# Kernel optimization log

Hardware: AMD Instinct MI355X
Metric: run time of the kernel (lower is better)

Reference implementation:

```python
import jax, jax.numpy as jnp
import numpy as np

B, T, TM, D, H, FF = 4, 1024, 1024, 1024, 16, 4096
HS = D // H
EPS = 1e-5


def _layer_norm(x, g, b):
    m = jnp.mean(x, axis=-1, keepdims=True)
    v = jnp.mean(jnp.square(x - m), axis=-1, keepdims=True)
    return (x - m) / jnp.sqrt(v + EPS) * g + b


def _mha(q_in, k_in, v_in, wq, bq, wk, bk, wv, bv, wo, bo):
    b, t, c = q_in.shape
    tm = k_in.shape[1]
    q = (q_in @ wq + bq).reshape(b, t, H, HS).transpose(0, 2, 1, 3)   # [b,h,t,hs]
    k = (k_in @ wk + bk).reshape(b, tm, H, HS).transpose(0, 2, 1, 3)  # [b,h,tm,hs]
    v = (v_in @ wv + bv).reshape(b, tm, H, HS).transpose(0, 2, 1, 3)
    att = jnp.einsum('bhtd,bhsd->bhts', q, k) * (1.0 / np.sqrt(HS))
    att = jax.nn.softmax(att, axis=-1)                                # [b,h,t,tm]
    y = jnp.einsum('bhts,bhsd->bhtd', att, v)
    y = y.transpose(0, 2, 1, 3).reshape(b, t, c)
    y = y @ wo + bo
    return y, att.mean(axis=1)                                        # attn avg over heads


def setup_inputs() -> dict:
    key = jax.random.key(0)
    ks = jax.random.split(key, 32)
    s = 0.02
    w = lambda k, shape: (jax.random.normal(k, shape, jnp.float32) * s)
    inp = {
        'tgt': jax.random.normal(ks[0], (B, T, D), jnp.float32),
        'memory': jax.random.normal(ks[1], (B, TM, D), jnp.float32),
        # self-attention params
        'sa_wq': w(ks[2], (D, D)), 'sa_bq': jnp.zeros((D,), jnp.float32),
        'sa_wk': w(ks[3], (D, D)), 'sa_bk': jnp.zeros((D,), jnp.float32),
        'sa_wv': w(ks[4], (D, D)), 'sa_bv': jnp.zeros((D,), jnp.float32),
        'sa_wo': w(ks[5], (D, D)), 'sa_bo': jnp.zeros((D,), jnp.float32),
        # cross-attention params
        'ca_wq': w(ks[6], (D, D)), 'ca_bq': jnp.zeros((D,), jnp.float32),
        'ca_wk': w(ks[7], (D, D)), 'ca_bk': jnp.zeros((D,), jnp.float32),
        'ca_wv': w(ks[8], (D, D)), 'ca_bv': jnp.zeros((D,), jnp.float32),
        'ca_wo': w(ks[9], (D, D)), 'ca_bo': jnp.zeros((D,), jnp.float32),
        # FFN
        'w1': w(ks[10], (D, FF)), 'b1': jnp.zeros((FF,), jnp.float32),
        'w2': w(ks[11], (FF, D)), 'b2': jnp.zeros((D,), jnp.float32),
        # LayerNorms
        'ln1_g': jnp.ones((D,), jnp.float32), 'ln1_b': jnp.zeros((D,), jnp.float32),
        'ln2_g': jnp.ones((D,), jnp.float32), 'ln2_b': jnp.zeros((D,), jnp.float32),
        'ln3_g': jnp.ones((D,), jnp.float32), 'ln3_b': jnp.zeros((D,), jnp.float32),
    }
    return inp


def reference(tgt, memory,
              sa_wq, sa_bq, sa_wk, sa_bk, sa_wv, sa_bv, sa_wo, sa_bo,
              ca_wq, ca_bq, ca_wk, ca_bk, ca_wv, ca_bv, ca_wo, ca_bo,
              w1, b1, w2, b2,
              ln1_g, ln1_b, ln2_g, ln2_b, ln3_g, ln3_b):
    x = tgt
    tmp, _ = _mha(x, x, x, sa_wq, sa_bq, sa_wk, sa_bk, sa_wv, sa_bv, sa_wo, sa_bo)
    x = _layer_norm(x + tmp, ln1_g, ln1_b)
    tmp, attention = _mha(x, memory, memory,
                          ca_wq, ca_bq, ca_wk, ca_bk, ca_wv, ca_bv, ca_wo, ca_bo)
    x = _layer_norm(x + tmp, ln2_g, ln2_b)
    tmp = jax.nn.relu(x @ w1 + b1) @ w2 + b2
    x = _layer_norm(x + tmp, ln3_g, ln3_b)
    return x, attention
```

## Files before the change

kernel.cpp:

```cpp
#include <hip/hip_runtime.h>
#include <hip/hip_bf16.h>
#include <cstdint>
#include <cstddef>

using u16 = unsigned short;
typedef __attribute__((ext_vector_type(4))) float f32x4;
typedef __attribute__((ext_vector_type(8))) short bf16x8;
typedef __attribute__((ext_vector_type(4))) short bf16x4;

constexpr int Bc = 4, Tc = 1024, TMc = 1024, Dc = 1024, Hc = 16, HSc = 64, FFc = 4096;
constexpr int BT = Bc * Tc;

struct Ptr4 { u16* p0; u16* p1; u16* p2; u16* p3; };

__device__ __forceinline__ u16 f2bf(float f) {
  union { float f; uint32_t u; } v; v.f = f;
  uint32_t u = v.u;
  u += 0x7fffu + ((u >> 16) & 1u);
  return (u16)(u >> 16);
}
__device__ __forceinline__ float b2f(u16 u) {
  union { float f; uint32_t u32; } v; v.u32 = (uint32_t)u << 16; return v.f;
}

__device__ __forceinline__ bf16x8 cat8(bf16x4 lo, bf16x4 hi) {
  bf16x8 r;
  r[0] = lo[0]; r[1] = lo[1]; r[2] = lo[2]; r[3] = lo[3];
  r[4] = hi[0]; r[5] = hi[1]; r[6] = hi[2]; r[7] = hi[3];
  return r;
}

__device__ __forceinline__ void gload16(const u16* g, u16* l) {
  __builtin_amdgcn_global_load_lds((const __attribute__((address_space(1))) void*)g,
                                   (__attribute__((address_space(3))) void*)l, 16, 0, 0);
}

__global__ __launch_bounds__(256)
void tconv(const float* __restrict__ in, u16* __restrict__ outp, int K, int N)
{
  __shared__ u16 tile[64][65];
  const int tx = threadIdx.x & 15, ty = threadIdx.x >> 4;
  const int kb = blockIdx.y * 64, nb = blockIdx.x * 64;
  #pragma unroll
  for (int i = 0; i < 4; ++i) {
    const int r = ty + i * 16;
    const float4 v = *(const float4*)(in + (size_t)(kb + r) * N + nb + tx * 4);
    tile[r][tx * 4 + 0] = f2bf(v.x);
    tile[r][tx * 4 + 1] = f2bf(v.y);
    tile[r][tx * 4 + 2] = f2bf(v.z);
    tile[r][tx * 4 + 3] = f2bf(v.w);
  }
  __syncthreads();
  #pragma unroll
  for (int i = 0; i < 4; ++i) {
    const int n = ty + i * 16;
    bf16x4 o;
    o[0] = (short)tile[tx * 4 + 0][n];
    o[1] = (short)tile[tx * 4 + 1][n];
    o[2] = (short)tile[tx * 4 + 2][n];
    o[3] = (short)tile[tx * 4 + 3][n];
    *(bf16x4*)(outp + (size_t)(nb + n) * K + kb + tx * 4) = o;
  }
}

__global__ __launch_bounds__(256)
void cvt_bf16(const float* __restrict__ in, u16* __restrict__ outp, int n4)
{
  const int i = blockIdx.x * 256 + threadIdx.x;
  if (i < n4) {
    const float4 v = ((const float4*)in)[i];
    bf16x4 o;
    o[0] = (short)f2bf(v.x); o[1] = (short)f2bf(v.y);
    o[2] = (short)f2bf(v.z); o[3] = (short)f2bf(v.w);
    ((bf16x4*)outp)[i] = o;
  }
}

template<int MODE, int BMv, int DEPTH>
__global__ __launch_bounds__((BMv == 256) ? 512 : 256)
void gemm_bt(const u16* __restrict__ A, const u16* __restrict__ Bt,
             const float* __restrict__ bias, const float* __restrict__ resid,
             void* __restrict__ outp, int M, int N, int K, int Kch, Ptr4 P)
{
  constexpr int BM = BMv, BN = 128, BK = 32;
  constexpr int NTHR = (BM == 256) ? 512 : 256;
  constexpr int RPC = NTHR / 4;
  constexpr int ACALLS = BM / RPC;
  constexpr int BCALLS = BN / RPC;
  constexpr int CALLS = ACALLS + BCALLS;
  constexpr int NB = DEPTH + 1;
  __shared__ __align__(16) u16 As[NB][BM * BK];
  __shared__ __align__(16) u16 Bs[NB][BN * BK];
  const int tid = threadIdx.x;
  const int lane = tid & 63, w = tid >> 6;
  const int wr = w >> 1, wc = w & 1;
  const int hi4 = lane >> 4, lr = lane & 15;

  const int nwg = gridDim.x;
  const int GX = N / BN;
  const int bid0 = (int)blockIdx.x;
  const int L = (bid0 & 7) * (nwg >> 3) + (bid0 >> 3);
  const int bandw = 8 * GX;
  const int band = L / bandw;
  const int rem = L - band * bandw;
  const int m0 = (band * 8 + (rem & 7)) * BM;
  const int n0 = (rem >> 3) * BN;

  const int k0 = (MODE == 3) ? (int)blockIdx.y * Kch : 0;

  const int srow = tid >> 2;
  const int gslot = (tid & 3) ^ ((srow >> 1) & 3);
  const u16* ga = A  + (size_t)(m0 + srow) * K + k0 + gslot * 8;
  const u16* gb = Bt + (size_t)(n0 + srow) * K + k0 + gslot * 8;
  const int wofs = w * 512;
  const int cswz = (lr >> 1) & 3;

  auto stage = [&](int buf, int kt) {
    #pragma unroll
    for (int j = 0; j < ACALLS; ++j)
      gload16(ga + (size_t)j * RPC * K + kt, &As[buf][j * NTHR * 8 + wofs]);
    #pragma unroll
    for (int j = 0; j < BCALLS; ++j)
      gload16(gb + (size_t)j * RPC * K + kt, &Bs[buf][j * NTHR * 8 + wofs]);
  };

  f32x4 acc[4][4] = {};
  const int nt = Kch / BK;

  #pragma unroll
  for (int p = 0; p < DEPTH; ++p)
    if (p < nt) stage(p % NB, p * BK);

  int cur = 0;
  for (int t = 0; t < nt; ++t) {
    {
      const int ahead = nt - 1 - t;
      const int cap = (ahead < DEPTH - 1 ? ahead : DEPTH - 1) * CALLS;
      switch (cap) {
        case 0:  asm volatile("s_waitcnt vmcnt(0)"  ::: "memory"); break;
        case 3:  asm volatile("s_waitcnt vmcnt(3)"  ::: "memory"); break;
        case 4:  asm volatile("s_waitcnt vmcnt(4)"  ::: "memory"); break;
        case 8:  asm volatile("s_waitcnt vmcnt(8)"  ::: "memory"); break;
        default: asm volatile("s_waitcnt vmcnt(12)" ::: "memory"); break;
      }
    }
    __builtin_amdgcn_s_barrier();
    __builtin_amdgcn_sched_barrier(0);

    if (t + DEPTH < nt) {
      int b2 = cur + DEPTH; if (b2 >= NB) b2 -= NB;
      stage(b2, (t + DEPTH) * BK);
    }

    bf16x8 af[4], bfr[4];
    #pragma unroll
    for (int mb = 0; mb < 4; ++mb)
      af[mb] = *(const bf16x8*)&As[cur][(wr * 64 + mb * 16 + lr) * BK + (hi4 ^ cswz) * 8];
    #pragma unroll
    for (int nb = 0; nb < 4; ++nb)
      bfr[nb] = *(const bf16x8*)&Bs[cur][(wc * 64 + nb * 16 + lr) * BK + (hi4 ^ cswz) * 8];
    #pragma unroll
    for (int mb = 0; mb < 4; ++mb)
      #pragma unroll
      for (int nb = 0; nb < 4; ++nb)
        acc[mb][nb] = __builtin_amdgcn_mfma_f32_16x16x32_bf16(af[mb], bfr[nb], acc[mb][nb], 0, 0, 0);

    ++cur; if (cur == NB) cur = 0;
  }

  const int orow = m0 + wr * 64 + 4 * hi4;
  const int ocol = n0 + wc * 64 + lr;

  if (MODE == 1) {
    #pragma unroll
    for (int nb = 0; nb < 4; ++nb) {
      const int c = ocol + nb * 16;
      const float bv = bias ? bias[c] : 0.0f;
      #pragma unroll
      for (int mb = 0; mb < 4; ++mb) {
        #pragma unroll
        for (int r = 0; r < 4; ++r) {
          const size_t idx = (size_t)(orow + mb * 16 + r) * N + c;
          ((float*)outp)[idx] = acc[mb][nb][r] + bv + resid[idx];
        }
      }
    }
  } else {
    __syncthreads();
    u16* eb = &Bs[0][0] + w * 1088;
    u16* pout_;
    if (MODE == 3) {
      const int sk = blockIdx.y;
      pout_ = (sk == 0) ? P.p0 : (sk == 1) ? P.p1 : (sk == 2) ? P.p2 : P.p3;
    } else {
      pout_ = (u16*)outp;
    }
    const int r2 = lane >> 3;
    const int c2 = (lane & 7) * 8;
    #pragma unroll
    for (int mb = 0; mb < 4; ++mb) {
      #pragma unroll
      for (int nb = 0; nb < 4; ++nb) {
        const int c = ocol + nb * 16;
        const float bv = (MODE != 3 && bias) ? bias[c] : 0.0f;
        #pragma unroll
        for (int r = 0; r < 4; ++r) {
          float v = acc[mb][nb][r] + bv;
          if (MODE == 2) v = fmaxf(v, 0.0f);
          eb[(4 * hi4 + r) * 68 + nb * 16 + lr] = f2bf(v);
        }
      }
      #pragma unroll
      for (int pass = 0; pass < 2; ++pass) {
        const int rr = pass * 8 + r2;
        const bf16x8 vv = *(const bf16x8*)&eb[rr * 68 + c2];
        *(bf16x8*)&pout_[(size_t)(m0 + wr * 64 + mb * 16 + rr) * N + n0 + wc * 64 + c2] = vv;
      }
    }
  }
}

__global__ __launch_bounds__(256)
void flash_attn(const u16* __restrict__ Q, const u16* __restrict__ Kb,
                const u16* __restrict__ Vb, u16* __restrict__ Y,
                float* __restrict__ Mout, float* __restrict__ Lout,
                int qstr, int kstr)
{
  constexpr int LDK = 72;
  __shared__ __align__(16) u16 Ks[64 * LDK];
  __shared__ __align__(16) u16 Vt[64 * LDK];
  const int tid = threadIdx.x, lane = tid & 63, w = tid >> 6;
  const int hi4 = lane >> 4, lr = lane & 15;
  const int bh = blockIdx.y, b = bh >> 4, h = bh & 15;
  const int q0 = blockIdx.x * 64 + w * 16;

  bf16x8 qf[2];
  {
    const u16* qp = Q + ((size_t)(b * Tc + q0 + lr)) * qstr + h * HSc;
    #pragma unroll
    for (int ks = 0; ks < 2; ++ks)
      qf[ks] = cat8(*(const bf16x4*)(qp + ks * 32 + 4 * hi4),
                    *(const bf16x4*)(qp + ks * 32 + 16 + 4 * hi4));
  }

  float m_run = -1e30f, l_run = 0.0f;
  f32x4 o[4] = {};

  const int krow = tid >> 3, kcol = (tid & 7) * 8;
  const int vs = tid >> 4, vd = (tid & 15) * 4;
  const int vswz = 4 * (tid & 15);

  for (int s0 = 0; s0 < TMc; s0 += 64) {
    const u16* kp = Kb + ((size_t)(b * TMc + s0 + krow)) * kstr + h * HSc + kcol;
    *(bf16x8*)&Ks[krow * LDK + kcol]        = *(const bf16x8*)kp;
    *(bf16x8*)&Ks[(krow + 32) * LDK + kcol] = *(const bf16x8*)(kp + (size_t)32 * kstr);
    #pragma unroll
    for (int rr = 0; rr < 4; ++rr) {
      const int ss = vs + rr * 16;
      bf16x4 vv = *(const bf16x4*)(Vb + ((size_t)(b * TMc + s0 + ss)) * kstr + h * HSc + vd);
      const int sc_ = ss ^ vswz;
      Vt[(vd + 0) * LDK + sc_] = (u16)vv[0];
      Vt[(vd + 1) * LDK + sc_] = (u16)vv[1];
      Vt[(vd + 2) * LDK + sc_] = (u16)vv[2];
      Vt[(vd + 3) * LDK + sc_] = (u16)vv[3];
    }
    __syncthreads();

    f32x4 st[4];
    #pragma unroll
    for (int kb2 = 0; kb2 < 4; ++kb2) {
      f32x4 a = {};
      #pragma unroll
      for (int ks = 0; ks < 2; ++ks) {
        const u16* p = &Ks[(kb2 * 16 + lr) * LDK + ks * 32 + 4 * hi4];
        bf16x8 kf = cat8(*(const bf16x4*)p, *(const bf16x4*)(p + 16));
        a = __builtin_amdgcn_mfma_f32_16x16x32_bf16(kf, qf[ks], a, 0, 0, 0);
      }
      st[kb2] = a;
    }

    float cmax = -1e30f;
    #pragma unroll
    for (int kb2 = 0; kb2 < 4; ++kb2)
      #pragma unroll
      for (int r = 0; r < 4; ++r) {
        st[kb2][r] *= 0.125f;
        cmax = fmaxf(cmax, st[kb2][r]);
      }
    cmax = fmaxf(cmax, __shfl_xor(cmax, 16));
    cmax = fmaxf(cmax, __shfl_xor(cmax, 32));
    const float m_new = fmaxf(m_run, cmax);
    const float sc = __expf(m_run - m_new);
    float psum = 0.0f;
    #pragma unroll
    for (int kb2 = 0; kb2 < 4; ++kb2)
      #pragma unroll
      for (int r = 0; r < 4; ++r) {
        const float e = __expf(st[kb2][r] - m_new);
        st[kb2][r] = e;
        psum += e;
      }
    psum += __shfl_xor(psum, 16);
    psum += __shfl_xor(psum, 32);
    l_run = l_run * sc + psum;
    m_run = m_new;

    #pragma unroll
    for (int r = 0; r < 4; ++r) {
      const float osc = __shfl(sc, 4 * hi4 + r);
      #pragma unroll
      for (int nb = 0; nb < 4; ++nb) o[nb][r] *= osc;
    }

    bf16x8 pa[2];
    #pragma unroll
    for (int ks = 0; ks < 2; ++ks) {
      bf16x8 t;
      #pragma unroll
      for (int i = 0; i < 4; ++i) t[i]     = (short)f2bf(st[2 * ks + 0][i]);
      #pragma unroll
      for (int i = 0; i < 4; ++i) t[4 + i] = (short)f2bf(st[2 * ks + 1][i]);
      pa[ks] = t;
    }
    #pragma unroll
    for (int nb = 0; nb < 4; ++nb) {
      const int row = nb * 16 + lr;
      const int g = 4 * (row >> 2);
      #pragma unroll
      for (int ks = 0; ks < 2; ++ks) {
        const int c0 = (ks * 32 + 4 * hi4) ^ g;
        const int c1 = (ks * 32 + 16 + 4 * hi4) ^ g;
        bf16x8 vf = cat8(*(const bf16x4*)&Vt[row * LDK + c0],
                         *(const bf16x4*)&Vt[row * LDK + c1]);
        o[nb] = __builtin_amdgcn_mfma_f32_16x16x32_bf16(pa[ks], vf, o[nb], 0, 0, 0);
      }
    }
    __syncthreads();
  }

  #pragma unroll
  for (int r = 0; r < 4; ++r) {
    const float li = 1.0f / __shfl(l_run, 4 * hi4 + r);
    const size_t yr = ((size_t)(b * Tc + q0 + 4 * hi4 + r)) * Dc + h * HSc;
    #pragma unroll
    for (int nb = 0; nb < 4; ++nb)
      Y[yr + nb * 16 + lr] = f2bf(o[nb][r] * li);
  }
  if (Mout != nullptr && lane < 16) {
    Mout[(size_t)bh * Tc + q0 + lr] = m_run;
    Lout[(size_t)bh * Tc + q0 + lr] = l_run;
  }
}

__global__ __launch_bounds__(256)
void attn_avg(const u16* __restrict__ Q, const u16* __restrict__ Kb,
              const float* __restrict__ Mws, const float* __restrict__ Lws,
              float* __restrict__ outp, int qstr, int kstr)
{
  __shared__ __align__(16) u16 Ks[2][64 * 64];
  __shared__ __align__(16) float avg[64 * 68];
  const int tid = threadIdx.x, lane = tid & 63, w = tid >> 6;
  const int hi4 = lane >> 4, lr = lane & 15;
  const int b = blockIdx.z, qt = blockIdx.y, scn = blockIdx.x;
  const int q0 = qt * 64 + w * 16;
  const int s0 = scn * 64;

  const int srow = w * 8 + (lane >> 3);
  const int scol = ((lane & 7) ^ (lane >> 3)) * 8;
  const u16* kg = Kb + ((size_t)(b * TMc + s0 + srow)) * kstr + scol;
  const size_t skip32 = (size_t)32 * kstr;

  auto stage = [&](int buf, int h) {
    const u16* g = kg + h * HSc;
    gload16(g,          &Ks[buf][w * 512]);
    gload16(g + skip32, &Ks[buf][2048 + w * 512]);
  };

  float acc[4][4] = {};
  const int rsw = lr & 7;

  stage(0, 0);
  #pragma unroll 1
  for (int h = 0; h < Hc; ++h) {
    const int cur = h & 1;
    __syncthreads();
    if (h + 1 < Hc) stage(cur ^ 1, h + 1);

    const u16* qp = Q + ((size_t)(b * Tc + q0 + lr)) * qstr + h * HSc;
    const bf16x8 qf0 = *(const bf16x8*)(qp + 8 * hi4);
    const bf16x8 qf1 = *(const bf16x8*)(qp + 32 + 8 * hi4);
    const float mh = Mws[(size_t)(b * Hc + h) * Tc + q0 + lr];
    const float li = 1.0f / Lws[(size_t)(b * Hc + h) * Tc + q0 + lr];

    #pragma unroll
    for (int kb2 = 0; kb2 < 4; ++kb2) {
      const int row = kb2 * 16 + lr;
      const bf16x8 kf0 = *(const bf16x8*)&Ks[cur][row * 64 + ((hi4     ) ^ rsw) * 8];
      const bf16x8 kf1 = *(const bf16x8*)&Ks[cur][row * 64 + ((hi4 + 4) ^ rsw) * 8];
      f32x4 a = {};
      a = __builtin_amdgcn_mfma_f32_16x16x32_bf16(kf0, qf0, a, 0, 0, 0);
      a = __builtin_amdgcn_mfma_f32_16x16x32_bf16(kf1, qf1, a, 0, 0, 0);
      #pragma unroll
      for (int r = 0; r < 4; ++r)
        acc[kb2][r] += __expf(a[r] * 0.125f - mh) * li;
    }
  }

  __syncthreads();
  #pragma unroll
  for (int kb2 = 0; kb2 < 4; ++kb2)
    #pragma unroll
    for (int r = 0; r < 4; ++r)
      avg[(w * 16 + lr) * 68 + kb2 * 16 + 4 * hi4 + r] = acc[kb2][r] * (1.0f / Hc);
  __syncthreads();
  const int row = tid >> 2, col = (tid & 3) * 16;
  float* gp = outp + ((size_t)(b * Tc + qt * 64 + row)) * TMc + s0 + col;
  #pragma unroll
  for (int j = 0; j < 4; ++j)
    *(f32x4*)(gp + j * 4) = *(const f32x4*)&avg[row * 68 + col + j * 4];
}

__global__ __launch_bounds__(256)
void add_ln(const float* __restrict__ in, const float* __restrict__ g,
            const float* __restrict__ bb, float* __restrict__ outf,
            u16* __restrict__ outb)
{
  __shared__ float red1[4];
  __shared__ float red2[4];
  const int tid = threadIdx.x, lane = tid & 63, w = tid >> 6;
  const size_t row = blockIdx.x;
  float4 v = ((const float4*)(in + row * Dc))[tid];
  float s = v.x + v.y + v.z + v.w;
  #pragma unroll
  for (int o = 32; o >= 1; o >>= 1) s += __shfl_xor(s, o);
  if (lane == 0) red1[w] = s;
  __syncthreads();
  s = red1[0] + red1[1] + red1[2] + red1[3];
  const float mean = s * (1.0f / Dc);
  const float dx = v.x - mean, dy = v.y - mean, dz = v.z - mean, dw = v.w - mean;
  float s2 = dx * dx + dy * dy + dz * dz + dw * dw;
  #pragma unroll
  for (int o = 32; o >= 1; o >>= 1) s2 += __shfl_xor(s2, o);
  if (lane == 0) red2[w] = s2;
  __syncthreads();
  s2 = red2[0] + red2[1] + red2[2] + red2[3];
  const float rstd = rsqrtf(s2 * (1.0f / Dc) + 1e-5f);
  const float4 gv = ((const float4*)g)[tid];
  const float4 bv = ((const float4*)bb)[tid];
  float4 o4;
  o4.x = dx * rstd * gv.x + bv.x;
  o4.y = dy * rstd * gv.y + bv.y;
  o4.z = dz * rstd * gv.z + bv.z;
  o4.w = dw * rstd * gv.w + bv.w;
  ((float4*)(outf + row * Dc))[tid] = o4;
  if (outb != nullptr) {
    bf16x4 ob;
    ob[0] = (short)f2bf(o4.x); ob[1] = (short)f2bf(o4.y);
    ob[2] = (short)f2bf(o4.z); ob[3] = (short)f2bf(o4.w);
    *(bf16x4*)(outb + row * Dc + (size_t)tid * 4) = ob;
  }
}

__global__ __launch_bounds__(256)
void add_ln4(const u16* __restrict__ p0, const u16* __restrict__ p1,
             const u16* __restrict__ p2, const u16* __restrict__ p3,
             const float* __restrict__ bias2, const float* __restrict__ resid,
             const float* __restrict__ g, const float* __restrict__ bb,
             float* __restrict__ outf)
{
  __shared__ float red1[4];
  __shared__ float red2[4];
  const int tid = threadIdx.x, lane = tid & 63, w = tid >> 6;
  const size_t row = blockIdx.x;
  const size_t base = row * Dc + (size_t)tid * 4;
  const bf16x4 a0 = *(const bf16x4*)(p0 + base);
  const bf16x4 a1 = *(const bf16x4*)(p1 + base);
  const bf16x4 a2 = *(const bf16x4*)(p2 + base);
  const bf16x4 a3 = *(const bf16x4*)(p3 + base);
  const float4 rv = ((const float4*)(resid + row * Dc))[tid];
  const float4 b2 = ((const float4*)bias2)[tid];
  float4 v;
  v.x = b2f((u16)a0[0]) + b2f((u16)a1[0]) + b2f((u16)a2[0]) + b2f((u16)a3[0]) + b2.x + rv.x;
  v.y = b2f((u16)a0[1]) + b2f((u16)a1[1]) + b2f((u16)a2[1]) + b2f((u16)a3[1]) + b2.y + rv.y;
  v.z = b2f((u16)a0[2]) + b2f((u16)a1[2]) + b2f((u16)a2[2]) + b2f((u16)a3[2]) + b2.z + rv.z;
  v.w = b2f((u16)a0[3]) + b2f((u16)a1[3]) + b2f((u16)a2[3]) + b2f((u16)a3[3]) + b2.w + rv.w;
  float s = v.x + v.y + v.z + v.w;
  #pragma unroll
  for (int o = 32; o >= 1; o >>= 1) s += __shfl_xor(s, o);
  if (lane == 0) red1[w] = s;
  __syncthreads();
  s = red1[0] + red1[1] + red1[2] + red1[3];
  const float mean = s * (1.0f / Dc);
  const float dx = v.x - mean, dy = v.y - mean, dz = v.z - mean, dw = v.w - mean;
  float s2 = dx * dx + dy * dy + dz * dz + dw * dw;
  #pragma unroll
  for (int o = 32; o >= 1; o >>= 1) s2 += __shfl_xor(s2, o);
  if (lane == 0) red2[w] = s2;
  __syncthreads();
  s2 = red2[0] + red2[1] + red2[2] + red2[3];
  const float rstd = rsqrtf(s2 * (1.0f / Dc) + 1e-5f);
  const float4 gv = ((const float4*)g)[tid];
  const float4 bv = ((const float4*)bb)[tid];
  float4 o4;
  o4.x = dx * rstd * gv.x + bv.x;
  o4.y = dy * rstd * gv.y + bv.y;
  o4.z = dz * rstd * gv.z + bv.z;
  o4.w = dw * rstd * gv.w + bv.w;
  ((float4*)(outf + row * Dc))[tid] = o4;
}

extern "C" void kernel_launch(void* const* d_in, const int* in_sizes, int n_in,
                              void* d_out, int out_size, void* d_ws, size_t ws_size,
                              hipStream_t stream)
{
  (void)in_sizes; (void)n_in; (void)out_size; (void)ws_size;
  const float* tgt = (const float*)d_in[0];
  const float* mem = (const float*)d_in[1];
  const float* Wf[10]   = { (const float*)d_in[2],  (const float*)d_in[4],  (const float*)d_in[6],  (const float*)d_in[8],
                            (const float*)d_in[10], (const float*)d_in[12], (const float*)d_in[14], (const float*)d_in[16],
                            (const float*)d_in[18], (const float*)d_in[20] };
  const float* bias_[10]= { (const float*)d_in[3],  (const float*)d_in[5],  (const float*)d_in[7],  (const float*)d_in[9],
                            (const float*)d_in[11], (const float*)d_in[13], (const float*)d_in[15], (const float*)d_in[17],
                            (const float*)d_in[19], (const float*)d_in[21] };
  const float* ln1g = (const float*)d_in[22]; const float* ln1b = (const float*)d_in[23];
  const float* ln2g = (const float*)d_in[24]; const float* ln2b = (const float*)d_in[25];
  const float* ln3g = (const float*)d_in[26]; const float* ln3b = (const float*)d_in[27];

  char* wsp = (char*)d_ws;
  auto alloc = [&](size_t bytes) -> char* {
    char* p = wsp;
    wsp += (bytes + 255) & ~(size_t)255;
    return p;
  };
  u16* wT[8];
  for (int i = 0; i < 8; ++i) wT[i] = (u16*)alloc((size_t)Dc * Dc * 2);
  u16* w1T  = (u16*)alloc((size_t)Dc * FFc * 2);
  u16* w2T  = (u16*)alloc((size_t)Dc * FFc * 2);
  u16* xb   = (u16*)alloc((size_t)BT * Dc * 2);
  u16* memb = (u16*)alloc((size_t)BT * Dc * 2);
  u16* qb   = (u16*)alloc((size_t)BT * Dc * 2);
  u16* yb   = (u16*)alloc((size_t)BT * Dc * 2);
  u16* ffb  = (u16*)alloc((size_t)BT * FFc * 2);
  float* res = (float*)alloc((size_t)BT * Dc * 4);
  float* xf  = (float*)alloc((size_t)BT * Dc * 4);
  float* mws = (float*)alloc((size_t)Bc * Hc * Tc * 4);
  float* lws = (float*)alloc((size_t)Bc * Hc * Tc * 4);
  float* bqkv = (float*)alloc(3 * Dc * 4);
  float* bkv  = (float*)alloc(2 * Dc * 4);

  u16* qkv    = ffb;
  u16* kvb    = ffb;
  u16* wqkvT  = (u16*)res;
  Ptr4 fp { qb, yb, memb, (u16*)res };

  float* out_x   = (float*)d_out;
  float* out_att = out_x + (size_t)BT * Dc;

  Ptr4 z { nullptr, nullptr, nullptr, nullptr };

  for (int i = 0; i < 8; ++i)
    tconv<<<dim3(Dc / 64, Dc / 64), 256, 0, stream>>>(Wf[i], wT[i], Dc, Dc);
  tconv<<<dim3(FFc / 64, Dc / 64), 256, 0, stream>>>(Wf[8], w1T, Dc, FFc);
  tconv<<<dim3(Dc / 64, FFc / 64), 256, 0, stream>>>(Wf[9], w2T, FFc, Dc);
  cvt_bf16<<<BT * Dc / 4 / 256, 256, 0, stream>>>(tgt, xb, BT * Dc / 4);
  cvt_bf16<<<BT * Dc / 4 / 256, 256, 0, stream>>>(mem, memb, BT * Dc / 4);

  for (int j = 0; j < 3; ++j) {
    hipMemcpyAsync(wqkvT + (size_t)j * Dc * Dc, wT[j], (size_t)Dc * Dc * 2,
                   hipMemcpyDeviceToDevice, stream);
    hipMemcpyAsync(bqkv + j * Dc, bias_[j], Dc * 4, hipMemcpyDeviceToDevice, stream);
  }
  for (int j = 0; j < 2; ++j)
    hipMemcpyAsync(bkv + j * Dc, bias_[5 + j], Dc * 4, hipMemcpyDeviceToDevice, stream);

  const int nD    = (Dc / 128) * (BT / 128);
  const int nQKVw = (3 * Dc / 128) * (BT / 256);
  const int nKVw  = (2 * Dc / 128) * (BT / 256);
  const int nFw   = (FFc / 128) * (BT / 256);
  const dim3 gAtt(Tc / 64, Bc * Hc);
  const dim3 gAvg(TMc / 64, Tc / 64, Bc);

  gemm_bt<0, 256, 2><<<nQKVw, 512, 0, stream>>>(xb, wqkvT, bqkv, nullptr, qkv, BT, 3 * Dc, Dc, Dc, z);
  flash_attn<<<gAtt, 256, 0, stream>>>(qkv, qkv + Dc, qkv + 2 * Dc, yb,
                                       nullptr, nullptr, 3 * Dc, 3 * Dc);
  gemm_bt<1, 128, 2><<<nD, 256, 0, stream>>>(yb, wT[3], bias_[3], tgt, res, BT, Dc, Dc, Dc, z);
  add_ln<<<BT, 256, 0, stream>>>(res, ln1g, ln1b, xf, xb);

  gemm_bt<0, 128, 2><<<nD, 256, 0, stream>>>(xb, wT[4], bias_[4], nullptr, qb, BT, Dc, Dc, Dc, z);
  gemm_bt<0, 256, 2><<<nKVw, 512, 0, stream>>>(memb, wT[5], bkv, nullptr, kvb, BT, 2 * Dc, Dc, Dc, z);
  flash_attn<<<gAtt, 256, 0, stream>>>(qb, kvb, kvb + Dc, yb, mws, lws, Dc, 2 * Dc);
  attn_avg<<<gAvg, 256, 0, stream>>>(qb, kvb, mws, lws, out_att, Dc, 2 * Dc);
  gemm_bt<1, 128, 2><<<nD, 256, 0, stream>>>(yb, wT[7], bias_[7], xf, res, BT, Dc, Dc, Dc, z);
  add_ln<<<BT, 256, 0, stream>>>(res, ln2g, ln2b, xf, xb);

  gemm_bt<2, 256, 2><<<nFw, 512, 0, stream>>>(xb,  w1T, bias_[8], nullptr, ffb, BT, FFc, Dc, Dc, z);
  gemm_bt<3, 128, 2><<<dim3(nD, 4), 256, 0, stream>>>(ffb, w2T, nullptr, nullptr, nullptr,
                                                      BT, Dc, FFc, FFc / 4, fp);
  add_ln4<<<BT, 256, 0, stream>>>(fp.p0, fp.p1, fp.p2, fp.p3, bias_[9], xf,
                                  ln3g, ln3b, out_x);
}
```

Measured before the change: 481.6 us.

## Double-buffer K/V tiles in flash attention with register prefetch

The flash attention loop now keeps two LDS buffers for K and transposed V. The next tile is prefetched into registers while the current tile is being computed, then written to the other buffer, so each iteration needs one barrier instead of two. The V transpose also changes: each thread gathers a 4x4 block and writes vectorized bf16x4 stores instead of scalar u16 stores. This doubles LDS use and raises register pressure, which may reduce occupancy.

```diff
diff --git a/kernel.cpp b/kernel.cpp
--- a/kernel.cpp
+++ b/kernel.cpp
@@ -227,8 +227,8 @@
                 int qstr, int kstr)
 {
   constexpr int LDK = 72;
-  __shared__ __align__(16) u16 Ks[64 * LDK];
-  __shared__ __align__(16) u16 Vt[64 * LDK];
+  __shared__ __align__(16) u16 Ks[2][64 * LDK];
+  __shared__ __align__(16) u16 Vt[2][64 * LDK];
   const int tid = threadIdx.x, lane = tid & 63, w = tid >> 6;
   const int hi4 = lane >> 4, lr = lane & 15;
   const int bh = blockIdx.y, b = bh >> 4, h = bh & 15;
@@ -247,24 +247,43 @@
   f32x4 o[4] = {};
 
   const int krow = tid >> 3, kcol = (tid & 7) * 8;
-  const int vs = tid >> 4, vd = (tid & 15) * 4;
-  const int vswz = 4 * (tid & 15);
-
-  for (int s0 = 0; s0 < TMc; s0 += 64) {
-    const u16* kp = Kb + ((size_t)(b * TMc + s0 + krow)) * kstr + h * HSc + kcol;
-    *(bf16x8*)&Ks[krow * LDK + kcol]        = *(const bf16x8*)kp;
-    *(bf16x8*)&Ks[(krow + 32) * LDK + kcol] = *(const bf16x8*)(kp + (size_t)32 * kstr);
-    #pragma unroll
-    for (int rr = 0; rr < 4; ++rr) {
-      const int ss = vs + rr * 16;
-      bf16x4 vv = *(const bf16x4*)(Vb + ((size_t)(b * TMc + s0 + ss)) * kstr + h * HSc + vd);
-      const int sc_ = ss ^ vswz;
-      Vt[(vd + 0) * LDK + sc_] = (u16)vv[0];
-      Vt[(vd + 1) * LDK + sc_] = (u16)vv[1];
-      Vt[(vd + 2) * LDK + sc_] = (u16)vv[2];
-      Vt[(vd + 3) * LDK + sc_] = (u16)vv[3];
-    }
+  const int s4 = (tid >> 4) * 4;
+  const int d4 = (tid & 15) * 4;
+
+  const u16* kbase = Kb + ((size_t)(b * TMc + krow)) * kstr + h * HSc + kcol;
+  const u16* vbase = Vb + ((size_t)(b * TMc + s4)) * kstr + h * HSc + d4;
+
+  bf16x8 kreg0, kreg1;
+  bf16x4 vreg[4];
+
+  auto loadch = [&](int s0) {
+    const u16* kp = kbase + (size_t)s0 * kstr;
+    kreg0 = *(const bf16x8*)kp;
+    kreg1 = *(const bf16x8*)(kp + (size_t)32 * kstr);
+    const u16* vp = vbase + (size_t)s0 * kstr;
+    #pragma unroll
+    for (int j = 0; j < 4; ++j)
+      vreg[j] = *(const bf16x4*)(vp + (size_t)j * kstr);
+  };
+  auto writech = [&](int buf) {
+    *(bf16x8*)&Ks[buf][krow * LDK + kcol]        = kreg0;
+    *(bf16x8*)&Ks[buf][(krow + 32) * LDK + kcol] = kreg1;
+    #pragma unroll
+    for (int i = 0; i < 4; ++i) {
+      bf16x4 tr;
+      tr[0] = vreg[0][i]; tr[1] = vreg[1][i]; tr[2] = vreg[2][i]; tr[3] = vreg[3][i];
+      *(bf16x4*)&Vt[buf][(d4 + i) * LDK + (s4 ^ d4)] = tr;
+    }
+  };
+
+  loadch(0);
+  writech(0);
+
+  constexpr int NT = TMc / 64;
+  for (int t = 0; t < NT; ++t) {
+    const int cur = t & 1;
     __syncthreads();
+    if (t + 1 < NT) loadch((t + 1) * 64);
 
     f32x4 st[4];
     #pragma unroll
@@ -272,7 +291,7 @@
       f32x4 a = {};
       #pragma unroll
       for (int ks = 0; ks < 2; ++ks) {
-        const u16* p = &Ks[(kb2 * 16 + lr) * LDK + ks * 32 + 4 * hi4];
+        const u16* p = &Ks[cur][(kb2 * 16 + lr) * LDK + ks * 32 + 4 * hi4];
         bf16x8 kf = cat8(*(const bf16x4*)p, *(const bf16x4*)(p + 16));
         a = __builtin_amdgcn_mfma_f32_16x16x32_bf16(kf, qf[ks], a, 0, 0, 0);
       }
@@ -315,12 +334,12 @@
     bf16x8 pa[2];
     #pragma unroll
     for (int ks = 0; ks < 2; ++ks) {
-      bf16x8 t;
-      #pragma unroll
-      for (int i = 0; i < 4; ++i) t[i]     = (short)f2bf(st[2 * ks + 0][i]);
-      #pragma unroll
-      for (int i = 0; i < 4; ++i) t[4 + i] = (short)f2bf(st[2 * ks + 1][i]);
-      pa[ks] = t;
+      bf16x8 tv;
+      #pragma unroll
+      for (int i = 0; i < 4; ++i) tv[i]     = (short)f2bf(st[2 * ks + 0][i]);
+      #pragma unroll
+      for (int i = 0; i < 4; ++i) tv[4 + i] = (short)f2bf(st[2 * ks + 1][i]);
+      pa[ks] = tv;
     }
     #pragma unroll
     for (int nb = 0; nb < 4; ++nb) {
@@ -330,12 +349,13 @@
       for (int ks = 0; ks < 2; ++ks) {
         const int c0 = (ks * 32 + 4 * hi4) ^ g;
         const int c1 = (ks * 32 + 16 + 4 * hi4) ^ g;
-        bf16x8 vf = cat8(*(const bf16x4*)&Vt[row * LDK + c0],
-                         *(const bf16x4*)&Vt[row * LDK + c1]);
+        bf16x8 vf = cat8(*(const bf16x4*)&Vt[cur][row * LDK + c0],
+                         *(const bf16x4*)&Vt[cur][row * LDK + c1]);
         o[nb] = __builtin_amdgcn_mfma_f32_16x16x32_bf16(pa[ks], vf, o[nb], 0, 0, 0);
       }
     }
-    __syncthreads();
+
+    if (t + 1 < NT) writech(cur ^ 1);
   }
 
   #pragma unroll
```

After: 454.9 us. 5.5% less time.
